# Kernel optimization log

Hardware: AMD Instinct MI355X
Metric: run time of the kernel (lower is better)

Reference implementation:

```python
import jax, jax.numpy as jnp
import numpy as np

B, H, W, IN, HID, L, M1, M2, OUT, NT = 32, 128, 256, 4, 64, 4, 12, 12, 2, 14


def setup_inputs() -> dict:
    key = jax.random.key(0)
    ks = jax.random.split(key, 32)
    f32 = jnp.float32
    n = lambda k, s, scale=0.02: jax.random.normal(k, s, dtype=f32) * scale
    inp = jax.random.normal(ks[0], (B, H, W, IN), dtype=f32)
    # ext: [B,1,6]; col0 float feature, col2 day idx in [0,8), col3 hour idx in [5,19)
    c0 = jax.random.uniform(ks[1], (B, 1), dtype=f32)
    c1 = jax.random.uniform(ks[2], (B, 1), dtype=f32)
    c2 = jax.random.randint(ks[3], (B, 1), 0, 8).astype(f32)
    c3 = jax.random.randint(ks[4], (B, 1), 5, 19).astype(f32)
    c45 = jax.random.uniform(ks[5], (B, 2), dtype=f32)
    ext = jnp.concatenate([c0, c1, c2, c3, c45], axis=1)[:, None, :]
    return {
        'inp': inp, 'ext': ext,
        'enc_w': n(ks[6], (HID, IN + 1)), 'enc_b': n(ks[7], (HID,)),
        'w1r': n(ks[8], (L, HID, HID, M1, M2), 1.0 / (HID * HID)),
        'w1i': n(ks[9], (L, HID, HID, M1, M2), 1.0 / (HID * HID)),
        'w2r': n(ks[10], (L, HID, HID, M1, M2), 1.0 / (HID * HID)),
        'w2i': n(ks[11], (L, HID, HID, M1, M2), 1.0 / (HID * HID)),
        'ws_w': n(ks[12], (L, HID, HID)), 'ws_b': n(ks[13], (L, HID)),
        'day_emb': n(ks[14], (8, 2), 1.0), 'hour_emb': n(ks[15], (24, 3), 1.0),
        'e1_w': n(ks[16], (64, 6)), 'e1_b': n(ks[17], (64,)),
        'e2_w': n(ks[18], (H * W, 64)), 'e2_b': n(ks[19], (H * W,)),
        'tw': n(ks[20], (NT, HID, HID, 3, 3)), 'tb': n(ks[21], (NT, HID)),
        'f1_w': n(ks[22], (128, HID)), 'f1_b': n(ks[23], (128,)),
        'f2_w': n(ks[24], (HID, 128)), 'f2_b': n(ks[25], (HID,)),
        'f3_w': n(ks[26], (OUT, HID)), 'f3_b': n(ks[27], (OUT,)),
    }


def _act(x):
    return jax.nn.gelu(x, approximate=False)  # torch nn.GELU default (erf)


def _spectral(x, w1, w2):
    # x: [b,c,h,w]; w1,w2: complex [c_in,c_out,M1,M2]
    b, c, h, w = x.shape
    xft = jnp.fft.rfft2(x)  # [b,c,h,w//2+1]
    out = jnp.zeros((b, w1.shape[1], h, w // 2 + 1), dtype=xft.dtype)
    out = out.at[:, :, :M1, :M2].set(
        jnp.einsum('bixy,ioxy->boxy', xft[:, :, :M1, :M2], w1))
    out = out.at[:, :, -M1:, :M2].set(
        jnp.einsum('bixy,ioxy->boxy', xft[:, :, -M1:, :M2], w2))
    return jnp.fft.irfft2(out, s=(h, w))


def reference(inp, ext, enc_w, enc_b, w1r, w1i, w2r, w2i, ws_w, ws_b,
              day_emb, hour_emb, e1_w, e1_b, e2_w, e2_b, tw, tb,
              f1_w, f1_b, f2_w, f2_b, f3_w, f3_b):
    b, h, w, _ = inp.shape
    e = ext[:, 0, :]  # squeeze(1) -> [b,6]
    # embed_ext: [ext0, day_emb, hour_emb] -> [b,6]
    emb = jnp.concatenate([
        e[:, 0:1],
        day_emb[e[:, 2].astype(jnp.int32)],
        hour_emb[e[:, 3].astype(jnp.int32)],
    ], axis=1)
    # ext2lr_global (dropout = identity in eval)
    g = _act(emb @ e1_w.T + e1_b)
    g = _act(g @ e2_w.T + e2_b).reshape(b, h, w, 1)
    x = jnp.concatenate([inp, g], axis=-1)          # [b,h,w,IN+1]
    x = (x @ enc_w.T + enc_b).transpose(0, 3, 1, 2)  # [b,HID,h,w]
    # FNO integral layers
    for i in range(L):
        x1 = _spectral(x, w1r[i] + 1j * w1i[i], w2r[i] + 1j * w2i[i])
        x2 = jnp.einsum('bchw,oc->bohw', x, ws_w[i]) + ws_b[i][None, :, None, None]
        x = x1 + x2
        if i != L - 1:
            x = _act(x)
    # decoder_time: per-sample expert conv selected by hour index
    t = e[:, 3].astype(jnp.int32) - 5  # in [0, NT)
    Wt, bt = tw[t], tb[t]              # [b,HID,HID,3,3], [b,HID]
    def one(xi, wi, bi):
        y = jax.lax.conv_general_dilated(
            xi[None], wi, (1, 1), 'SAME',
            dimension_numbers=('NCHW', 'OIHW', 'NCHW'))[0]
        return y + bi[:, None, None]
    hfeat = _act(jax.vmap(one)(x, Wt, bt)).transpose(0, 2, 3, 1)  # [b,h,w,HID]
    # decoder MLP
    z = _act(hfeat @ f1_w.T + f1_b)
    z = _act(z @ f2_w.T + f2_b)
    return z @ f3_w.T + f3_b  # [b,h,w,OUT]
```

## Files before the change

### kernel.cpp

```cpp
#include <hip/hip_runtime.h>
#include <math.h>

#define BB 32
#define HH_ 128
#define WW_ 256

typedef _Float16 f16_t;
typedef _Float16 half8 __attribute__((ext_vector_type(8)));
typedef _Float16 half4 __attribute__((ext_vector_type(4)));
typedef float floatx4 __attribute__((ext_vector_type(4)));

__device__ __forceinline__ float gelu_f(float v){
  return 0.5f * v * (1.0f + erff(v * 0.70710678118654752f));
}

__global__ void k_diag(float* out, float v){ out[threadIdx.x] = v; }

__global__ __launch_bounds__(256) void k_prep(
      float2* twf, float2* thf, float2* thi, f16_t* twzh,
      const float* __restrict__ f1_w, const float* __restrict__ f2_w,
      const float* __restrict__ f3_w, f16_t* f1T, f16_t* f2T, f16_t* f3T,
      const float* __restrict__ tw, f16_t* __restrict__ wT,
      const float* __restrict__ w1r, const float* __restrict__ w1i,
      const float* __restrict__ w2r, const float* __restrict__ w2i,
      float2* __restrict__ wmix, f16_t* __restrict__ twA){
  __shared__ __align__(16) char smp[53248];
  const double PI2 = 6.283185307179586476925286766559;
  int blk = blockIdx.x, tid = threadIdx.x;
  if (blk < 113){
    int t = blk*256 + tid;
    if (t < 3072){
      int w = t/12, ky = t%12;
      double a = -PI2 * (double)(w*ky) / 256.0;
      twf[t] = make_float2((float)cos(a), (float)sin(a));
    } else if (t < 6144){
      int f = t-3072; int h = f/24, j = f%24;
      int kx = (j<12)? j : j+104;
      double a = -PI2 * (double)(h*kx) / 128.0;
      thf[f] = make_float2((float)cos(a), (float)sin(a));
    } else if (t < 9216){
      int f = t-6144; int h = f/24, j = f%24;
      int kx = (j<12)? j : j+104;
      double a = PI2 * (double)(h*kx) / 128.0;
      thi[f] = make_float2((float)(cos(a)/128.0), (float)(sin(a)/128.0));
    } else if (t < 12288){
      int f = t-9216; int w = f/12, ky = f%12;
      double a = PI2 * (double)(w*ky) / 256.0;
      double s = (ky==0)? 1.0 : 2.0;
      twzh[w*32 + ky]      = (f16_t)( s*cos(a)/256.0);
      twzh[w*32 + 12 + ky] = (f16_t)(-s*sin(a)/256.0);
      if (ky < 8) twzh[w*32 + 24 + ky] = (f16_t)0.f;
    } else {
      int t2 = t - 12288;
      if (t2 < 8192) f1T[t2] = (f16_t)f1_w[t2];
      else if (t2 < 16384) f2T[t2-8192] = (f16_t)f2_w[t2-8192];
      else if (t2 < 16512) f3T[t2-16384] = (f16_t)f3_w[t2-16384];
    }
  } else if (blk < 169){
    float* s = (float*)smp;
    int b2 = blk - 113;
    int og = b2 & 3, tt = b2 >> 2;
    const float* src = tw + (long)tt*36864 + og*9216;
    for (int f = tid; f < 9216; f += 256) s[f] = src[f];
    __syncthreads();
    for (int f = tid; f < 9216; f += 256){
      int c = f & 63; int r = f >> 6;
      int o16 = r % 16, tap = r / 16;
      float v = s[(o16*64 + c)*9 + tap];
      wT[(((long)tt*9 + tap)*64 + og*16 + o16)*64 + c] = (f16_t)v;
    }
  } else if (blk < 937){
    float* sr = (float*)smp;
    float* si = (float*)(smp + 26624);
    int b2 = blk - 169;
    int ig  = b2 & 7;
    int kx  = (b2 >> 3) % 12;
    int sel = (b2 / 96) & 1;
    int l   = b2 / 192;
    const float* wr = sel ? w2r : w1r;
    const float* wi = sel ? w2i : w1i;
    for (int f = tid; f < 6144; f += 256){
      int i8 = f / 768; int rem = f % 768;
      int o = rem / 12, ky = rem % 12;
      long addr = (((long)l*64 + ig*8 + i8)*64 + o)*144 + kx*12 + ky;
      sr[(i8*64 + o)*13 + ky] = wr[addr];
      si[(i8*64 + o)*13 + ky] = wi[addr];
    }
    __syncthreads();
    int j = sel ? (kx + 12) : kx;
    for (int f = tid; f < 6144; f += 256){
      int o = f & 63; int r = f >> 6;
      int ky = r % 12, i8 = r / 12;
      int sidx = (i8*64 + o)*13 + ky;
      wmix[(((long)l*288 + j*12 + ky))*4096 + (ig*8 + i8)*64 + o] =
          make_float2(sr[sidx], si[sidx]);
    }
  } else {
    int t = (blk - 937)*256 + tid;
    int halfi = t >> 13, r = t & 8191;
    int hl = r >> 12, r2 = r & 4095;
    int m = r2 >> 7, k = r2 & 127;
    f16_t v = (f16_t)0.f;
    if (m < 24){
      int ky = m >> 1, ri = m & 1;
      int w = halfi*128 + k;
      double a = -PI2 * (double)(w*ky) / 256.0;
      float t32 = (float)(ri ? sin(a) : cos(a));
      f16_t hi = (f16_t)t32;
      v = hl ? (f16_t)(t32 - (float)hi) : hi;
    }
    twA[t] = v;
  }
}

__global__ __launch_bounds__(256) void k_gx(const float* __restrict__ ext,
      const float* __restrict__ day_emb, const float* __restrict__ hour_emb,
      const float* __restrict__ e1_w, const float* __restrict__ e1_b,
      const float* __restrict__ e2_w, const float* __restrict__ e2_b,
      const float* __restrict__ inp, const float* __restrict__ enc_w,
      const float* __restrict__ enc_b, f16_t* __restrict__ x){
  int b = blockIdx.y;
  int hw = blockIdx.x*256 + threadIdx.x;
  __shared__ float s[64];
  __shared__ float ew[320];
  __shared__ float eb[64];
  if (threadIdx.x < 64){
    int j = threadIdx.x;
    const float* e = ext + b*6;
    float emb[6];
    emb[0] = e[0];
    int d  = (int)e[2];
    emb[1] = day_emb[d*2];  emb[2] = day_emb[d*2+1];
    int hr = (int)e[3];
    emb[3] = hour_emb[hr*3]; emb[4] = hour_emb[hr*3+1]; emb[5] = hour_emb[hr*3+2];
    float acc = e1_b[j];
    #pragma unroll
    for (int k = 0; k < 6; k++) acc += emb[k]*e1_w[j*6+k];
    s[j] = gelu_f(acc);
    eb[j] = enc_b[j];
  }
  for (int f = threadIdx.x; f < 320; f += 256) ew[f] = enc_w[f];
  __syncthreads();
  const float4* wrow = (const float4*)(e2_w + (long)hw*64);
  float acc = e2_b[hw];
  #pragma unroll
  for (int k = 0; k < 16; k++){
    float4 v = wrow[k];
    acc += v.x*s[4*k] + v.y*s[4*k+1] + v.z*s[4*k+2] + v.w*s[4*k+3];
  }
  float gv = gelu_f(acc);
  long pix = (long)b*(HH_*WW_) + hw;
  float4 ip = *(const float4*)(inp + pix*4);
  f16_t* xp = x + pix*64;
  #pragma unroll
  for (int c8 = 0; c8 < 8; c8++){
    half8 hv;
    #pragma unroll
    for (int e = 0; e < 8; e++){
      int c = c8*8 + e;
      const float* wr2 = ew + c*5;
      hv[e] = (f16_t)(eb[c] + ip.x*wr2[0] + ip.y*wr2[1] + ip.z*wr2[2]
                      + ip.w*wr2[3] + gv*wr2[4]);
    }
    *(half8*)(xp + c8*8) = hv;
  }
}

__global__ __launch_bounds__(256) void k_dft_w(const f16_t* __restrict__ x,
      const float4* __restrict__ twf4, float2* __restrict__ fft1){
  __shared__ float4 tw[1536];
  for (int f = threadIdx.x; f < 1536; f += 256) tw[f] = twf4[f];
  __syncthreads();
  int wave = threadIdx.x >> 6, lane = threadIdx.x & 63;
  long row = (long)blockIdx.x*4 + wave;
  const f16_t* xr = x + row*16384 + lane;
  float ar[12], ai[12];
  #pragma unroll
  for (int k = 0; k < 12; k++){ ar[k] = 0.f; ai[k] = 0.f; }
  for (int w = 0; w < 256; w++){
    float xv = (float)xr[(long)w*64];
    const float4* t = &tw[w*6];
    #pragma unroll
    for (int k = 0; k < 6; k++){
      float4 tv = t[k];
      ar[2*k]   += xv*tv.x;  ai[2*k]   += xv*tv.y;
      ar[2*k+1] += xv*tv.z;  ai[2*k+1] += xv*tv.w;
    }
  }
  float2* op = fft1 + row*768 + lane;
  #pragma unroll
  for (int ky = 0; ky < 12; ky++) op[ky*64] = make_float2(ar[ky], ai[ky]);
}

__global__ __launch_bounds__(256) void k_spec(const float2* __restrict__ s0,
      const float2* __restrict__ s1, int dual, const float2* __restrict__ thf_g,
      const float2* __restrict__ thi_g, const float2* __restrict__ wmix,
      int layer, float2* __restrict__ zi){
  __shared__ __align__(16) char sm[40960];
  float2* th  = (float2*)sm;
  float2* xch = (float2*)(sm + 24576);
  float2* mixL= (float2*)(sm + 24576);
  int tid = threadIdx.x;
  int b = blockIdx.x / 12, ky = blockIdx.x % 12;
  int wv = tid >> 6, lane = tid & 63;
  for (int f = tid; f < 3072; f += 256) th[f] = thf_g[f];
  float2 acc[6];
  #pragma unroll
  for (int q = 0; q < 6; q++) acc[q] = make_float2(0.f, 0.f);
  long base = (long)b*98304 + ky*64;
  for (int ch = 0; ch < 4; ch++){
    __syncthreads();
    for (int f = tid; f < 2048; f += 256){
      int hh = f >> 6, c = f & 63;
      long idx = base + (long)(ch*32 + hh)*768 + c;
      float2 v = s0[idx];
      if (dual){ float2 u = s1[idx]; v.x += u.x; v.y += u.y; }
      xch[f] = v;
    }
    __syncthreads();
    for (int hh = 0; hh < 32; hh++){
      float2 v = xch[hh*64 + lane];
      int hg = ch*32 + hh;
      #pragma unroll
      for (int q = 0; q < 6; q++){
        float2 t = th[hg*24 + q*4 + wv];
        acc[q].x += t.x*v.x - t.y*v.y;
        acc[q].y += t.x*v.y + t.y*v.x;
      }
    }
  }
  __syncthreads();
  for (int f = tid; f < 3072; f += 256) th[f] = thi_g[f];
  float2 mout[6];
  #pragma unroll
  for (int q = 0; q < 6; q++){
    int j = q*4 + wv;
    const float2* wj = wmix + (((long)layer*288 + j*12 + ky))*4096;
    float re = 0.f, im = 0.f;
    #pragma unroll 8
    for (int i = 0; i < 64; i++){
      float vr = __shfl(acc[q].x, i);
      float vi = __shfl(acc[q].y, i);
      float2 ww = wj[i*64 + lane];
      re += vr*ww.x - vi*ww.y;
      im += vr*ww.y + vi*ww.x;
    }
    mout[q] = make_float2(re, im);
  }
  #pragma unroll
  for (int q = 0; q < 6; q++) mixL[(q*4 + wv)*64 + lane] = mout[q];
  __syncthreads();
  float2 cr[24];
  #pragma unroll
  for (int j = 0; j < 24; j++) cr[j] = mixL[j*64 + lane];
  for (int qq = 0; qq < 32; qq++){
    int h = qq*4 + wv;
    float re = 0.f, im = 0.f;
    #pragma unroll
    for (int j = 0; j < 24; j++){
      float2 t = th[h*24 + j];
      re += t.x*cr[j].x - t.y*cr[j].y;
      im += t.x*cr[j].y + t.y*cr[j].x;
    }
    zi[((long)b*128 + h)*768 + ky*64 + lane] = make_float2(re, im);
  }
}

__global__ __launch_bounds__(256) void k_iw_mfma(f16_t* __restrict__ x,
      const float2* __restrict__ zi, const float* __restrict__ ws_w,
      const float* __restrict__ ws_b, const f16_t* __restrict__ twzh,
      const f16_t* __restrict__ twA, float2* __restrict__ fp0,
      float2* __restrict__ fp1, int layer, int act, int dodft){
  __shared__ __align__(16) char sm[52736];
  f16_t* A  = (f16_t*)sm;
  f16_t* Bm = (f16_t*)(sm + 34816);
  float* sb = (float*)(sm + 52224);
  f16_t* Obt  = (f16_t*)sm;
  f16_t* twA_l= (f16_t*)(sm + 17408);
  int tid = threadIdx.x;
  int blk = blockIdx.x;
  int half = blk & 1;
  long bh = blk >> 1;
  int w0 = half*128;
  const f16_t* xrow = x + (bh*256 + w0)*64;
  for (int f = tid; f < 1024; f += 256){
    int px = f >> 3, c8 = (f & 7)*8;
    *(float4*)((char*)A + (px*136 + c8)*2) = *(const float4*)(xrow + px*64 + c8);
  }
  for (int f = tid; f < 4096; f += 256){
    int px = f >> 5, k = f & 31;
    if (k < 24){
      f16_t v = twzh[(w0+px)*32 + k];
      A[px*136 + 64 + k] = v;
      A[px*136 + 88 + k] = v;
      A[px*136 + 112 + k] = (f16_t)0.f;
    }
  }
  const float* wsl = ws_w + (long)layer*4096;
  for (int f = tid; f < 1024; f += 256){
    int o = f >> 4, c4 = f & 15;
    float4 v = *(const float4*)(wsl + o*64 + c4*4);
    f16_t* d = Bm + o*136 + c4*4;
    d[0]=(f16_t)v.x; d[1]=(f16_t)v.y; d[2]=(f16_t)v.z; d[3]=(f16_t)v.w;
  }
  const float2* zrow = zi + bh*768;
  for (int f = tid; f < 768; f += 256){
    int o = f & 63, ky = f >> 6;
    float2 v = zrow[ky*64 + o];
    f16_t hr = (f16_t)v.x; f16_t hi_ = (f16_t)v.y;
    Bm[o*136 + 64 + ky] = hr;
    Bm[o*136 + 76 + ky] = hi_;
    Bm[o*136 + 88 + ky] = (f16_t)(v.x - (float)hr);
    Bm[o*136 +100 + ky] = (f16_t)(v.y - (float)hi_);
  }
  for (int f = tid; f < 2048; f += 256){
    int o = f >> 5, k = f & 31;
    if (k < 24) Bm[o*136 + 112 + k] = (f16_t)0.f;
  }
  if (tid < 64) sb[tid] = ws_b[layer*64 + tid];
  __syncthreads();
  int lane = tid & 63, wv = tid >> 6;
  int n15 = lane & 15, quad = lane >> 4;
  int n = wv*16 + n15;
  half8 bfr[4];
  #pragma unroll
  for (int kc = 0; kc < 4; kc++)
    bfr[kc] = *(const half8*)(Bm + n*136 + kc*32 + quad*8);
  floatx4 acc[8];
  #pragma unroll
  for (int mt = 0; mt < 8; mt++){
    floatx4 c = {0.f,0.f,0.f,0.f};
    #pragma unroll
    for (int kc = 0; kc < 4; kc++){
      half8 a = *(const half8*)(A + (mt*16 + n15)*136 + kc*32 + quad*8);
      c = __builtin_amdgcn_mfma_f32_16x16x32_f16(a, bfr[kc], c, 0, 0, 0);
    }
    acc[mt] = c;
  }
  float bias = sb[n];
  __syncthreads();
  f16_t* xo = x + (bh*256 + w0)*64;
  #pragma unroll
  for (int mt = 0; mt < 8; mt++){
    half4 hv;
    #pragma unroll
    for (int r = 0; r < 4; r++){
      float v = acc[mt][r] + bias;
      if (act) v = gelu_f(v);
      hv[r] = (f16_t)v;
      xo[(mt*16 + quad*4 + r)*64 + n] = hv[r];
    }
    if (dodft) *(half4*)(Obt + n*136 + mt*16 + quad*4) = hv;
  }
  if (dodft){
    const f16_t* tsrc = twA + half*8192;
    for (int f = tid; f < 1024; f += 256){
      int hl = f >> 9, m = (f >> 4) & 31, kc8 = f & 15;
      *(float4*)(twA_l + hl*4352 + m*136 + kc8*8) = *(const float4*)(tsrc + f*8);
    }
    __syncthreads();
    half8 bfr2[4];
    #pragma unroll
    for (int ks = 0; ks < 4; ks++)
      bfr2[ks] = *(const half8*)(Obt + n*136 + ks*32 + quad*8);
    floatx4 dacc[2];
    dacc[0] = (floatx4){0.f,0.f,0.f,0.f};
    dacc[1] = (floatx4){0.f,0.f,0.f,0.f};
    #pragma unroll
    for (int hl = 0; hl < 2; hl++){
      #pragma unroll
      for (int mt = 0; mt < 2; mt++){
        #pragma unroll
        for (int ks = 0; ks < 4; ks++){
          half8 a = *(const half8*)(twA_l + hl*4352 + (mt*16 + n15)*136
                                    + ks*32 + quad*8);
          dacc[mt] = __builtin_amdgcn_mfma_f32_16x16x32_f16(a, bfr2[ks],
                                                            dacc[mt], 0,0,0);
        }
      }
    }
    float2* dst = half ? fp1 : fp0;
    #pragma unroll
    for (int mt = 0; mt < 2; mt++){
      int m0 = mt*16 + quad*4;
      if (m0 < 24){
        int ky0 = m0 >> 1;
        dst[bh*768 + ky0*64 + n]     = make_float2(dacc[mt][0], dacc[mt][1]);
        dst[bh*768 + (ky0+1)*64 + n] = make_float2(dacc[mt][2], dacc[mt][3]);
      }
    }
  }
}

__global__ __launch_bounds__(256) void k_conv_head(const f16_t* __restrict__ x,
      const float* __restrict__ ext, const f16_t* __restrict__ wT,
      const float* __restrict__ tb, const f16_t* __restrict__ f1T,
      const float* __restrict__ f1_b, const f16_t* __restrict__ f2T,
      const float* __restrict__ f2_b, const f16_t* __restrict__ f3T,
      const float* __restrict__ f3_b, float* __restrict__ out){
  __shared__ __align__(16) char sm[37632];
  f16_t* hf   = (f16_t*)sm;
  f16_t* z1   = (f16_t*)(sm + 9216);
  f16_t* z2   = (f16_t*)(sm + 26624);
  float* tbs  = (float*)(sm + 35840);
  float* f1bs = (float*)(sm + 36096);
  float* f2bs = (float*)(sm + 36608);
  f16_t* f3s  = (f16_t*)(sm + 36864);
  float* f3bs = (float*)(sm + 37120);
  f16_t* xt   = (f16_t*)sm;

  int tid = threadIdx.x;
  int blk = blockIdx.x;
  int wc = blk & 3, h = (blk >> 2) & 127, b = blk >> 9;
  int w0 = wc*64;
  int t_idx = (int)ext[b*6+3] - 5;

  if (tid < 64) tbs[tid] = tb[t_idx*64 + tid];
  else if (tid < 192) f1bs[tid-64] = f1_b[tid-64];
  else f2bs[tid-192] = f2_b[tid-192];
  if (tid < 128) f3s[tid] = f3T[tid];
  if (tid < 2) f3bs[tid] = f3_b[tid];

  for (int f = tid; f < 3168; f += 256){
    int c4 = f & 15, r = f >> 4;
    int dy = r/66, pxl = r%66;
    int hh = h - 1 + dy, wg = w0 - 1 + pxl;
    ushort4 v = {0,0,0,0};
    if (hh >= 0 && hh < HH_ && wg >= 0 && wg < WW_)
      v = *(const ushort4*)(x + (((long)b*HH_ + hh)*WW_ + wg)*64 + c4*4);
    *(ushort4*)((unsigned short*)xt + (dy*66 + pxl)*72 + c4*4) = v;
  }
  __syncthreads();

  int lane = tid & 63, wv = tid >> 6;
  int n15 = lane & 15, quad = lane >> 4;

  floatx4 acc[4];
  #pragma unroll
  for (int mt = 0; mt < 4; mt++) acc[mt] = (floatx4){0.f,0.f,0.f,0.f};
  const f16_t* wTt = wT + (long)t_idx*36864;
  for (int tap = 0; tap < 9; tap++){
    int dy = tap/3, dx = tap%3;
    const f16_t* wrow = wTt + (tap*64 + wv*16 + n15)*64;
    #pragma unroll
    for (int kc = 0; kc < 2; kc++){
      half8 bfrag = *(const half8*)(wrow + kc*32 + quad*8);
      #pragma unroll
      for (int mt = 0; mt < 4; mt++){
        int p = mt*16 + n15 + dx;
        half8 a = *(const half8*)(xt + (dy*66 + p)*72 + kc*32 + quad*8);
        acc[mt] = __builtin_amdgcn_mfma_f32_16x16x32_f16(a, bfrag, acc[mt], 0,0,0);
      }
    }
  }
  __syncthreads();
  {
    int n = wv*16 + n15;
    float bias = tbs[n];
    #pragma unroll
    for (int mt = 0; mt < 4; mt++){
      #pragma unroll
      for (int r = 0; r < 4; r++){
        int m = mt*16 + quad*4 + r;
        hf[m*72 + n] = (f16_t)gelu_f(acc[mt][r] + bias);
      }
    }
  }
  __syncthreads();
  #pragma unroll
  for (int nt = 0; nt < 2; nt++){
    int n = wv*32 + nt*16 + n15;
    float bias = f1bs[n];
    half8 bf0 = *(const half8*)(f1T + n*64 + quad*8);
    half8 bf1 = *(const half8*)(f1T + n*64 + 32 + quad*8);
    #pragma unroll
    for (int mt = 0; mt < 4; mt++){
      floatx4 c = {0.f,0.f,0.f,0.f};
      half8 a0 = *(const half8*)(hf + (mt*16 + n15)*72 + quad*8);
      half8 a1 = *(const half8*)(hf + (mt*16 + n15)*72 + 32 + quad*8);
      c = __builtin_amdgcn_mfma_f32_16x16x32_f16(a0, bf0, c, 0,0,0);
      c = __builtin_amdgcn_mfma_f32_16x16x32_f16(a1, bf1, c, 0,0,0);
      #pragma unroll
      for (int r = 0; r < 4; r++){
        int m = mt*16 + quad*4 + r;
        z1[m*136 + n] = (f16_t)gelu_f(c[r] + bias);
      }
    }
  }
  __syncthreads();
  {
    int n = wv*16 + n15;
    float bias = f2bs[n];
    half8 bf[4];
    #pragma unroll
    for (int kc = 0; kc < 4; kc++)
      bf[kc] = *(const half8*)(f2T + n*128 + kc*32 + quad*8);
    #pragma unroll
    for (int mt = 0; mt < 4; mt++){
      floatx4 c = {0.f,0.f,0.f,0.f};
      #pragma unroll
      for (int kc = 0; kc < 4; kc++){
        half8 a = *(const half8*)(z1 + (mt*16 + n15)*136 + kc*32 + quad*8);
        c = __builtin_amdgcn_mfma_f32_16x16x32_f16(a, bf[kc], c, 0,0,0);
      }
      #pragma unroll
      for (int r = 0; r < 4; r++){
        int m = mt*16 + quad*4 + r;
        z2[m*72 + n] = (f16_t)gelu_f(c[r] + bias);
      }
    }
  }
  __syncthreads();
  if (tid < 128){
    int px = tid >> 1, oo = tid & 1;
    const f16_t* zr = z2 + px*72;
    const f16_t* fr = f3s + oo*64;
    float a = f3bs[oo];
    #pragma unroll
    for (int g = 0; g < 8; g++){
      half8 zv = *(const half8*)(zr + g*8);
      half8 wv2 = *(const half8*)(fr + g*8);
      #pragma unroll
      for (int q = 0; q < 8; q++) a += (float)zv[q]*(float)wv2[q];
    }
    out[(((long)b*HH_ + h)*WW_ + w0 + px)*2 + oo] = a;
  }
}

extern "C" void kernel_launch(void* const* d_in, const int* in_sizes, int n_in,
                              void* d_out, int out_size, void* d_ws, size_t ws_size,
                              hipStream_t stream){
  const float* inp     = (const float*)d_in[0];
  const float* ext     = (const float*)d_in[1];
  const float* enc_w   = (const float*)d_in[2];
  const float* enc_b   = (const float*)d_in[3];
  const float* w1r     = (const float*)d_in[4];
  const float* w1i     = (const float*)d_in[5];
  const float* w2r     = (const float*)d_in[6];
  const float* w2i     = (const float*)d_in[7];
  const float* ws_w    = (const float*)d_in[8];
  const float* ws_b    = (const float*)d_in[9];
  const float* day_emb = (const float*)d_in[10];
  const float* hour_emb= (const float*)d_in[11];
  const float* e1_w    = (const float*)d_in[12];
  const float* e1_b    = (const float*)d_in[13];
  const float* e2_w    = (const float*)d_in[14];
  const float* e2_b    = (const float*)d_in[15];
  const float* tw      = (const float*)d_in[16];
  const float* tb      = (const float*)d_in[17];
  const float* f1_w    = (const float*)d_in[18];
  const float* f1_b    = (const float*)d_in[19];
  const float* f2_w    = (const float*)d_in[20];
  const float* f2_b    = (const float*)d_in[21];
  const float* f3_w    = (const float*)d_in[22];
  const float* f3_b    = (const float*)d_in[23];
  float* outp = (float*)d_out;

  const size_t need = 248652032;
  if (ws_size < need){
    k_diag<<<dim3(1), dim3(64), 0, stream>>>(outp, (float)(ws_size >> 20));
    return;
  }
  char* p = (char*)d_ws;
  f16_t*  x    = (f16_t*)(p);
  float2* fp0  = (float2*)(p + 134217728);
  float2* fp1  = (float2*)(p + 159383552);
  float2* zi   = (float2*)(p + 184549376);
  float2* twf  = (float2*)(p + 209715200);
  float2* thf  = (float2*)(p + 209739776);
  float2* thi  = (float2*)(p + 209764352);
  f16_t*  twzh = (f16_t*)(p + 209788928);
  f16_t*  wT   = (f16_t*)(p + 209805312);
  f16_t*  f1T  = (f16_t*)(p + 210837504);
  f16_t*  f2T  = (f16_t*)(p + 210853888);
  f16_t*  f3T  = (f16_t*)(p + 210870272);
  float2* wmix = (float2*)(p + 210870528);
  f16_t*  twA  = (f16_t*)(p + 248619264);

  k_prep<<<dim3(1001), dim3(256), 0, stream>>>(twf, thf, thi, twzh,
      f1_w, f2_w, f3_w, f1T, f2T, f3T, tw, wT, w1r, w1i, w2r, w2i, wmix, twA);
  k_gx<<<dim3(128, 32), dim3(256), 0, stream>>>(ext, day_emb, hour_emb,
      e1_w, e1_b, e2_w, e2_b, inp, enc_w, enc_b, x);
  k_dft_w<<<dim3(1024), dim3(256), 0, stream>>>(x, (const float4*)twf, fp0);
  for (int l = 0; l < 4; l++){
    k_spec<<<dim3(384), dim3(256), 0, stream>>>(fp0, fp1, (l > 0) ? 1 : 0,
                                                thf, thi, wmix, l, zi);
    k_iw_mfma<<<dim3(8192), dim3(256), 0, stream>>>(x, zi, ws_w, ws_b, twzh,
                       twA, fp0, fp1, l, (l < 3) ? 1 : 0, (l < 3) ? 1 : 0);
  }
  k_conv_head<<<dim3(16384), dim3(256), 0, stream>>>(x, ext, wT, tb,
                     f1T, f1_b, f2T, f2_b, f3T, f3_b, outp);
}
```

Measured before the change: 1.404 ms.

## Fuse encoder lift with MFMA-based W-direction DFT and widen conv-head loads

Merges the global-embedding/encoder kernel and the scalar W-direction DFT kernel into one kernel per (batch,row). Each block keeps the freshly computed row in LDS and runs the truncated DFT with f16 MFMA using split hi/lo twiddles, writing into the two-buffer layout (fp0/fp1) that later layers already use, so k_spec now always runs in dual mode. This removes one launch and the re-read of x for the first DFT, and replaces FMA-bound scalar DFT work with matrix instructions. It also widens the conv-head halo loads from 8-byte to 16-byte vectors. The risks are larger LDS use (about 58 KB per block), which limits occupancy, and strided per-element global stores of x.

```diff
diff --git a/kernel.cpp b/kernel.cpp
--- a/kernel.cpp
+++ b/kernel.cpp
@@ -113,19 +113,26 @@
   }
 }
 
-__global__ __launch_bounds__(256) void k_gx(const float* __restrict__ ext,
+__global__ __launch_bounds__(256) void k_gxdft(const float* __restrict__ ext,
       const float* __restrict__ day_emb, const float* __restrict__ hour_emb,
       const float* __restrict__ e1_w, const float* __restrict__ e1_b,
       const float* __restrict__ e2_w, const float* __restrict__ e2_b,
       const float* __restrict__ inp, const float* __restrict__ enc_w,
-      const float* __restrict__ enc_b, f16_t* __restrict__ x){
-  int b = blockIdx.y;
-  int hw = blockIdx.x*256 + threadIdx.x;
-  __shared__ float s[64];
-  __shared__ float ew[320];
-  __shared__ float eb[64];
-  if (threadIdx.x < 64){
-    int j = threadIdx.x;
+      const float* __restrict__ enc_b, const f16_t* __restrict__ twA,
+      f16_t* __restrict__ x, float2* __restrict__ fp0, float2* __restrict__ fp1){
+  __shared__ __align__(16) char sm[59392];
+  f16_t* Obt   = (f16_t*)sm;
+  f16_t* twA_l = (f16_t*)(sm + 35072);
+  float* gvs   = (float*)(sm + 52480);
+  float4* ips  = (float4*)(sm + 53504);
+  float* s     = (float*)(sm + 57600);
+  float* ew    = (float*)(sm + 57856);
+  float* eb    = (float*)(sm + 59136);
+  int tid = threadIdx.x;
+  int bh = blockIdx.x;
+  int b = bh >> 7, h = bh & 127;
+  if (tid < 64){
+    int j = tid;
     const float* e = ext + b*6;
     float emb[6];
     emb[0] = e[0];
@@ -139,57 +146,94 @@
     s[j] = gelu_f(acc);
     eb[j] = enc_b[j];
   }
-  for (int f = threadIdx.x; f < 320; f += 256) ew[f] = enc_w[f];
-  __syncthreads();
-  const float4* wrow = (const float4*)(e2_w + (long)hw*64);
-  float acc = e2_b[hw];
-  #pragma unroll
-  for (int k = 0; k < 16; k++){
-    float4 v = wrow[k];
-    acc += v.x*s[4*k] + v.y*s[4*k+1] + v.z*s[4*k+2] + v.w*s[4*k+3];
-  }
-  float gv = gelu_f(acc);
-  long pix = (long)b*(HH_*WW_) + hw;
-  float4 ip = *(const float4*)(inp + pix*4);
-  f16_t* xp = x + pix*64;
-  #pragma unroll
-  for (int c8 = 0; c8 < 8; c8++){
-    half8 hv;
-    #pragma unroll
-    for (int e = 0; e < 8; e++){
-      int c = c8*8 + e;
-      const float* wr2 = ew + c*5;
-      hv[e] = (f16_t)(eb[c] + ip.x*wr2[0] + ip.y*wr2[1] + ip.z*wr2[2]
-                      + ip.w*wr2[3] + gv*wr2[4]);
-    }
-    *(half8*)(xp + c8*8) = hv;
-  }
-}
-
-__global__ __launch_bounds__(256) void k_dft_w(const f16_t* __restrict__ x,
-      const float4* __restrict__ twf4, float2* __restrict__ fft1){
-  __shared__ float4 tw[1536];
-  for (int f = threadIdx.x; f < 1536; f += 256) tw[f] = twf4[f];
-  __syncthreads();
-  int wave = threadIdx.x >> 6, lane = threadIdx.x & 63;
-  long row = (long)blockIdx.x*4 + wave;
-  const f16_t* xr = x + row*16384 + lane;
-  float ar[12], ai[12];
-  #pragma unroll
-  for (int k = 0; k < 12; k++){ ar[k] = 0.f; ai[k] = 0.f; }
-  for (int w = 0; w < 256; w++){
-    float xv = (float)xr[(long)w*64];
-    const float4* t = &tw[w*6];
-    #pragma unroll
-    for (int k = 0; k < 6; k++){
-      float4 tv = t[k];
-      ar[2*k]   += xv*tv.x;  ai[2*k]   += xv*tv.y;
-      ar[2*k+1] += xv*tv.z;  ai[2*k+1] += xv*tv.w;
-    }
-  }
-  float2* op = fft1 + row*768 + lane;
-  #pragma unroll
-  for (int ky = 0; ky < 12; ky++) op[ky*64] = make_float2(ar[ky], ai[ky]);
+  for (int f = tid; f < 320; f += 256) ew[f] = enc_w[f];
+  __syncthreads();
+  {
+    int px = tid;
+    long hw = (long)h*256 + px;
+    const float4* wrow = (const float4*)(e2_w + hw*64);
+    float acc = e2_b[hw];
+    #pragma unroll
+    for (int k = 0; k < 16; k++){
+      float4 v = wrow[k];
+      acc += v.x*s[4*k] + v.y*s[4*k+1] + v.z*s[4*k+2] + v.w*s[4*k+3];
+    }
+    gvs[px] = gelu_f(acc);
+    ips[px] = *(const float4*)(inp + ((long)b*32768 + hw)*4);
+  }
+  __syncthreads();
+  int lane = tid & 63, wv = tid >> 6;
+  {
+    int c = lane, wg = wv;
+    const float* wr2 = ew + c*5;
+    float w0 = wr2[0], w1 = wr2[1], w2 = wr2[2], w3 = wr2[3], w4 = wr2[4];
+    float ebc = eb[c];
+    f16_t* xo = x + ((long)bh*256 + wg*64)*64 + c;
+    #pragma unroll 2
+    for (int g8 = 0; g8 < 8; g8++){
+      half8 hv;
+      #pragma unroll
+      for (int e2 = 0; e2 < 8; e2++){
+        int i = g8*8 + e2;
+        float4 ip = ips[wg*64 + i];
+        float gv = gvs[wg*64 + i];
+        float v = ebc + ip.x*w0 + ip.y*w1 + ip.z*w2 + ip.w*w3 + gv*w4;
+        f16_t hval = (f16_t)v;
+        hv[e2] = hval;
+        xo[i*64] = hval;
+      }
+      *(half8*)(Obt + c*274 + wg*64 + g8*8) = hv;
+    }
+  }
+  for (int f = tid; f < 1024; f += 256){
+    int hl = f >> 9, m = (f >> 4) & 31, kc8 = f & 15;
+    *(float4*)(twA_l + hl*4352 + m*136 + kc8*8) = *(const float4*)(twA + f*8);
+  }
+  __syncthreads();
+  int n15 = lane & 15, quad = lane >> 4;
+  int n = wv*16 + n15;
+  #pragma unroll
+  for (int half = 0; half < 2; half++){
+    if (half == 1){
+      __syncthreads();
+      for (int f = tid; f < 1024; f += 256){
+        int hl = f >> 9, m = (f >> 4) & 31, kc8 = f & 15;
+        *(float4*)(twA_l + hl*4352 + m*136 + kc8*8) =
+            *(const float4*)(twA + 8192 + f*8);
+      }
+      __syncthreads();
+    }
+    half8 bfr2[4];
+    #pragma unroll
+    for (int ks = 0; ks < 4; ks++)
+      bfr2[ks] = *(const half8*)(Obt + n*274 + half*128 + ks*32 + quad*8);
+    floatx4 dacc[2];
+    dacc[0] = (floatx4){0.f,0.f,0.f,0.f};
+    dacc[1] = (floatx4){0.f,0.f,0.f,0.f};
+    #pragma unroll
+    for (int hl = 0; hl < 2; hl++){
+      #pragma unroll
+      for (int mt = 0; mt < 2; mt++){
+        #pragma unroll
+        for (int ks = 0; ks < 4; ks++){
+          half8 a = *(const half8*)(twA_l + hl*4352 + (mt*16 + n15)*136
+                                    + ks*32 + quad*8);
+          dacc[mt] = __builtin_amdgcn_mfma_f32_16x16x32_f16(a, bfr2[ks],
+                                                            dacc[mt], 0,0,0);
+        }
+      }
+    }
+    float2* dst = half ? fp1 : fp0;
+    #pragma unroll
+    for (int mt = 0; mt < 2; mt++){
+      int m0 = mt*16 + quad*4;
+      if (m0 < 24){
+        int ky0 = m0 >> 1;
+        dst[(long)bh*768 + ky0*64 + n]     = make_float2(dacc[mt][0], dacc[mt][1]);
+        dst[(long)bh*768 + (ky0+1)*64 + n] = make_float2(dacc[mt][2], dacc[mt][3]);
+      }
+    }
+  }
 }
 
 __global__ __launch_bounds__(256) void k_spec(const float2* __restrict__ s0,
@@ -421,14 +465,14 @@
   if (tid < 128) f3s[tid] = f3T[tid];
   if (tid < 2) f3bs[tid] = f3_b[tid];
 
-  for (int f = tid; f < 3168; f += 256){
-    int c4 = f & 15, r = f >> 4;
+  for (int f = tid; f < 1584; f += 256){
+    int c8 = f & 7, r = f >> 3;
     int dy = r/66, pxl = r%66;
     int hh = h - 1 + dy, wg = w0 - 1 + pxl;
-    ushort4 v = {0,0,0,0};
+    float4 v = {0.f,0.f,0.f,0.f};
     if (hh >= 0 && hh < HH_ && wg >= 0 && wg < WW_)
-      v = *(const ushort4*)(x + (((long)b*HH_ + hh)*WW_ + wg)*64 + c4*4);
-    *(ushort4*)((unsigned short*)xt + (dy*66 + pxl)*72 + c4*4) = v;
+      v = *(const float4*)(x + (((long)b*HH_ + hh)*WW_ + wg)*64 + c8*8);
+    *(float4*)(xt + (dy*66 + pxl)*72 + c8*8) = v;
   }
   __syncthreads();
 
@@ -579,11 +623,10 @@
 
   k_prep<<<dim3(1001), dim3(256), 0, stream>>>(twf, thf, thi, twzh,
       f1_w, f2_w, f3_w, f1T, f2T, f3T, tw, wT, w1r, w1i, w2r, w2i, wmix, twA);
-  k_gx<<<dim3(128, 32), dim3(256), 0, stream>>>(ext, day_emb, hour_emb,
-      e1_w, e1_b, e2_w, e2_b, inp, enc_w, enc_b, x);
-  k_dft_w<<<dim3(1024), dim3(256), 0, stream>>>(x, (const float4*)twf, fp0);
+  k_gxdft<<<dim3(4096), dim3(256), 0, stream>>>(ext, day_emb, hour_emb,
+      e1_w, e1_b, e2_w, e2_b, inp, enc_w, enc_b, twA, x, fp0, fp1);
   for (int l = 0; l < 4; l++){
-    k_spec<<<dim3(384), dim3(256), 0, stream>>>(fp0, fp1, (l > 0) ? 1 : 0,
+    k_spec<<<dim3(384), dim3(256), 0, stream>>>(fp0, fp1, 1,
                                                 thf, thi, wmix, l, zi);
     k_iw_mfma<<<dim3(8192), dim3(256), 0, stream>>>(x, zi, ws_w, ws_b, twzh,
                        twA, fp0, fp1, l, (l < 3) ? 1 : 0, (l < 3) ? 1 : 0);
```

Result: faster. 1.329 ms (-5.4%).
